# Performance work log

Measured on AMD Instinct MI355X. Metric: run time of the kernel, lower is better.

## Reference

```python
import jax, jax.numpy as jnp
import numpy as np

NUM_EXPERTS = 8
TOP_K = 2
N_EMBD = 1024
FF_HIDDEN = 4096


def setup_inputs() -> dict:
    key = jax.random.key(0)
    ks = jax.random.split(key, 5)
    scale = 0.02
    inputs = jax.random.normal(ks[0], (4, 2048, N_EMBD), dtype=jnp.float32)
    # torch Linear weights: (out_features, in_features)
    wg = jax.random.normal(ks[1], (NUM_EXPERTS, N_EMBD), dtype=jnp.float32) * scale
    w1 = jax.random.normal(ks[2], (NUM_EXPERTS, FF_HIDDEN, N_EMBD), dtype=jnp.float32) * scale
    w2 = jax.random.normal(ks[3], (NUM_EXPERTS, N_EMBD, FF_HIDDEN), dtype=jnp.float32) * scale
    w3 = jax.random.normal(ks[4], (NUM_EXPERTS, FF_HIDDEN, N_EMBD), dtype=jnp.float32) * scale
    return {"inputs": inputs, "wg": wg, "w1": w1, "w2": w2, "w3": w3}


def reference(inputs, wg, w1, w2, w3):
    B, S, D = inputs.shape
    xs = inputs.reshape(-1, D)                      # [T, D]
    T = xs.shape[0]
    E = wg.shape[0]
    gate_logits = xs @ wg.T                          # [T, E]
    top_w, sel = jax.lax.top_k(gate_logits, TOP_K)   # [T, K]
    top_w = jax.nn.softmax(top_w.astype(jnp.float32), axis=-1).astype(inputs.dtype)
    # scatter top-k weights into dense per-expert combine weights [T, E]
    combine = jnp.zeros((T, E), dtype=inputs.dtype)
    combine = combine.at[jnp.arange(T)[:, None], sel].set(top_w)
    out = jnp.zeros_like(xs)
    for e in range(E):  # small fixed loop over experts (structurally distinct weights)
        h = jax.nn.silu(xs @ w1[e].T) * (xs @ w3[e].T)   # [T, H]
        out = out + combine[:, e:e + 1] * (h @ w2[e].T)  # [T, D]
    return out.reshape(B, S, D)
```

## Files before the change

### kernel.cpp

```cpp
#include <hip/hip_runtime.h>
#include <math.h>

#define NEXP 8
#define TTOK 8192
#define DEMB 1024
#define HFF  4096

#define OFF_CNT   0
#define OFF_OFFS  64
#define OFF_PTOK  1024
#define OFF_PW    (OFF_PTOK + NEXP*TTOK*4)
#define OFF_XB    (OFF_PW + NEXP*TTOK*4)
#define OFF_WB    (OFF_XB + (size_t)TTOK*DEMB*2)

typedef short bf16x8 __attribute__((ext_vector_type(8)));
typedef float f32x4 __attribute__((ext_vector_type(4)));

__device__ __forceinline__ unsigned short f2bf(float f) {
  union { float f; unsigned int u; } v; v.f = f;
  unsigned int r = v.u + 0x7fffu + ((v.u >> 16) & 1u);
  return (unsigned short)(r >> 16);
}

__device__ __forceinline__ void gll16(const void* g, void* l) {
  __builtin_amdgcn_global_load_lds(
      (const __attribute__((address_space(1))) unsigned int*)g,
      (__attribute__((address_space(3))) unsigned int*)l, 16, 0, 0);
}

__global__ void k_convert_w(const float* __restrict__ w, uint4* __restrict__ wb) {
  size_t i = (size_t)blockIdx.x * 256 + threadIdx.x;
  float4 a = ((const float4*)w)[2 * i];
  float4 b = ((const float4*)w)[2 * i + 1];
  uint4 o;
  o.x = (unsigned)f2bf(a.x) | ((unsigned)f2bf(a.y) << 16);
  o.y = (unsigned)f2bf(a.z) | ((unsigned)f2bf(a.w) << 16);
  o.z = (unsigned)f2bf(b.x) | ((unsigned)f2bf(b.y) << 16);
  o.w = (unsigned)f2bf(b.z) | ((unsigned)f2bf(b.w) << 16);
  wb[i] = o;
}

__global__ __launch_bounds__(256) void k_gate(
    const float* __restrict__ x, const float* __restrict__ wg,
    int* __restrict__ cnt, int* __restrict__ ptok, float* __restrict__ pw,
    unsigned short* __restrict__ xb) {
  __shared__ float wgs[NEXP * DEMB];
  int tid = threadIdx.x;
  for (int i = tid; i < NEXP * DEMB / 4; i += 256)
    ((float4*)wgs)[i] = ((const float4*)wg)[i];
  __syncthreads();
  int lane = tid & 63;
  int t = blockIdx.x * 4 + (tid >> 6);
  const float* xr = x + (size_t)t * DEMB;
  unsigned short* xbr = xb + (size_t)t * DEMB;
  float acc[NEXP];
#pragma unroll
  for (int e = 0; e < NEXP; ++e) acc[e] = 0.f;
#pragma unroll
  for (int j = 0; j < 4; ++j) {
    int d = j * 256 + lane * 4;
    float4 v = *(const float4*)(xr + d);
    ushort4 o;
    o.x = f2bf(v.x); o.y = f2bf(v.y); o.z = f2bf(v.z); o.w = f2bf(v.w);
    *(ushort4*)(xbr + d) = o;
#pragma unroll
    for (int e = 0; e < NEXP; ++e) {
      float4 w = *(const float4*)(wgs + e * DEMB + d);
      acc[e] += v.x * w.x + v.y * w.y + v.z * w.z + v.w * w.w;
    }
  }
#pragma unroll
  for (int e = 0; e < NEXP; ++e) {
#pragma unroll
    for (int off = 32; off > 0; off >>= 1) acc[e] += __shfl_xor(acc[e], off);
  }
  if (lane == 0) {
    float b0 = -1e30f; int i0 = 0;
#pragma unroll
    for (int e = 0; e < NEXP; ++e) if (acc[e] > b0) { b0 = acc[e]; i0 = e; }
    float b1 = -1e30f; int i1 = 0;
#pragma unroll
    for (int e = 0; e < NEXP; ++e) if (e != i0 && acc[e] > b1) { b1 = acc[e]; i1 = e; }
    float ex = expf(b1 - b0);
    float s  = 1.f + ex;
    float w0 = 1.f / s;
    float w1v = ex / s;
    int s0 = atomicAdd(&cnt[i0], 1);
    ptok[i0 * TTOK + s0] = t; pw[i0 * TTOK + s0] = w0;
    int s1 = atomicAdd(&cnt[i1], 1);
    ptok[i1 * TTOK + s1] = t; pw[i1 * TTOK + s1] = w1v;
  }
}

__global__ void k_scan(const int* __restrict__ cnt, int* __restrict__ offs) {
  if (threadIdx.x == 0) {
    int s = 0;
    for (int e = 0; e < NEXP; ++e) { offs[e] = s; s += cnt[e]; }
  }
}


__global__ __launch_bounds__(256, 2) void k_gemm1(
    const unsigned short* __restrict__ Xb, const unsigned short* __restrict__ w1b,
    const unsigned short* __restrict__ w3b, const int* __restrict__ cnt,
    const int* __restrict__ offs, const int* __restrict__ ptok,
    unsigned short* __restrict__ Hb, int e_sel, int mbase, int mTiles) {
  int nwg = gridDim.x;
  int orig = blockIdx.x;
  int idp = (orig & 7) * (nwg >> 3) + (orig >> 3);
  int mt, e, nt;
  if (e_sel >= 0) { e = e_sel; mt = idp % mTiles; nt = idp / mTiles; }
  else { mt = idp % mTiles; e = (idp / mTiles) % NEXP; nt = idp / (mTiles * NEXP); }
  int ce = cnt[e];
  int m0 = mbase + mt * 128;
  if (m0 >= ce) return;
  int n0 = nt * 128;
  int hb = (e_sel >= 0) ? -mbase : offs[e];
  size_t eo = (size_t)((e_sel >= 0) ? 0 : e) * HFF * DEMB;
  const unsigned short* w1e = w1b + eo;
  const unsigned short* w3e = w3b + eo;

  __shared__ __align__(16) unsigned char sm[49152];
  unsigned char* As = sm;
  unsigned char* B1 = sm + 16384;
  unsigned char* B3 = sm + 32768;

  int tid = threadIdx.x, lane = tid & 63, wid = tid >> 6;
  int wm = (wid >> 1) * 64, wn = (wid & 1) * 64;

  const unsigned short *as[4], *b1s[4], *b3s[4];
#pragma unroll
  for (int it = 0; it < 4; ++it) {
    int c = it * 256 + tid;
    int row = c >> 3;
    int col = ((c & 7) ^ (row & 7)) * 8;
    int slot = m0 + row; slot = slot < ce ? slot : ce - 1;
    int tok = ptok[e * TTOK + slot];
    as[it]  = Xb + (size_t)tok * DEMB + col;
    b1s[it] = w1e + (size_t)(n0 + row) * DEMB + col;
    b3s[it] = w3e + (size_t)(n0 + row) * DEMB + col;
  }

  const f32x4 zf = {0.f, 0.f, 0.f, 0.f};
  f32x4 au[4][4], av[4][4];
#pragma unroll
  for (int a = 0; a < 4; ++a)
#pragma unroll
    for (int b = 0; b < 4; ++b) { au[a][b] = zf; av[a][b] = zf; }

  for (int kt = 0; kt < DEMB / 64; ++kt) {
    int k0 = kt * 64;
#pragma unroll
    for (int it = 0; it < 4; ++it) gll16(as[it] + k0,  As + it * 4096 + wid * 1024);
#pragma unroll
    for (int it = 0; it < 4; ++it) gll16(b1s[it] + k0, B1 + it * 4096 + wid * 1024);
#pragma unroll
    for (int it = 0; it < 4; ++it) gll16(b3s[it] + k0, B3 + it * 4096 + wid * 1024);
    __syncthreads();
#pragma unroll
    for (int kk = 0; kk < 64; kk += 32) {
      bf16x8 af[4], b1f[4], b3f[4];
      int kg = (kk >> 3) + (lane >> 4);
#pragma unroll
      for (int mr = 0; mr < 4; ++mr) {
        int r = wm + mr * 16 + (lane & 15);
        af[mr] = *(const bf16x8*)(As + r * 128 + ((kg ^ (r & 7)) * 16));
      }
#pragma unroll
      for (int nr = 0; nr < 4; ++nr) {
        int c = wn + nr * 16 + (lane & 15);
        int boff = c * 128 + ((kg ^ (c & 7)) * 16);
        b1f[nr] = *(const bf16x8*)(B1 + boff);
        b3f[nr] = *(const bf16x8*)(B3 + boff);
      }
#pragma unroll
      for (int mr = 0; mr < 4; ++mr)
#pragma unroll
        for (int nr = 0; nr < 4; ++nr) {
          au[mr][nr] = __builtin_amdgcn_mfma_f32_16x16x32_bf16(af[mr], b1f[nr], au[mr][nr], 0, 0, 0);
          av[mr][nr] = __builtin_amdgcn_mfma_f32_16x16x32_bf16(af[mr], b3f[nr], av[mr][nr], 0, 0, 0);
        }
    }
    __syncthreads();
  }
#pragma unroll
  for (int mr = 0; mr < 4; ++mr) {
#pragma unroll
    for (int j = 0; j < 4; ++j) {
      int rs = m0 + wm + mr * 16 + (lane >> 4) * 4 + j;
      if (rs < ce) {
        unsigned short* hrow = Hb + (size_t)(hb + rs) * HFF + n0 + wn + (lane & 15);
#pragma unroll
        for (int nr = 0; nr < 4; ++nr) {
          float u = au[mr][nr][j], v = av[mr][nr][j];
          float h = v * (u / (1.f + __expf(-u)));
          hrow[nr * 16] = f2bf(h);
        }
      }
    }
  }
}

__global__ __launch_bounds__(256, 2) void k_gemm2(
    const unsigned short* __restrict__ Hb, const unsigned short* __restrict__ w2b,
    const int* __restrict__ cnt, const int* __restrict__ offs,
    const int* __restrict__ ptok, const float* __restrict__ pw,
    float* __restrict__ out, int e_sel, int mbase, int mTiles) {
  int nwg = gridDim.x;
  int orig = blockIdx.x;
  int idp = (orig & 7) * (nwg >> 3) + (orig >> 3);
  int mt, e, nt;
  if (e_sel >= 0) { e = e_sel; mt = idp % mTiles; nt = idp / mTiles; }
  else { mt = idp % mTiles; e = (idp / mTiles) % NEXP; nt = idp / (mTiles * NEXP); }
  int ce = cnt[e];
  int m0 = mbase + mt * 128;
  if (m0 >= ce) return;
  int n0 = nt * 128;
  int hb = (e_sel >= 0) ? -mbase : offs[e];
  size_t eo = (size_t)((e_sel >= 0) ? 0 : e) * DEMB * HFF;
  const unsigned short* w2e = w2b + eo;

  __shared__ __align__(16) unsigned char sm[32768];
  unsigned char* As = sm;
  unsigned char* B2 = sm + 16384;

  int tid = threadIdx.x, lane = tid & 63, wid = tid >> 6;
  int wm = (wid >> 1) * 64, wn = (wid & 1) * 64;

  const unsigned short *as[4], *b2s[4];
#pragma unroll
  for (int it = 0; it < 4; ++it) {
    int c = it * 256 + tid;
    int row = c >> 3;
    int col = ((c & 7) ^ (row & 7)) * 8;
    int slot = m0 + row; slot = slot < ce ? slot : ce - 1;
    as[it]  = Hb + (size_t)(hb + slot) * HFF + col;
    b2s[it] = w2e + (size_t)(n0 + row) * HFF + col;
  }

  const f32x4 zf = {0.f, 0.f, 0.f, 0.f};
  f32x4 acc[4][4];
#pragma unroll
  for (int a = 0; a < 4; ++a)
#pragma unroll
    for (int b = 0; b < 4; ++b) acc[a][b] = zf;

  for (int kt = 0; kt < HFF / 64; ++kt) {
    int k0 = kt * 64;
#pragma unroll
    for (int it = 0; it < 4; ++it) gll16(as[it] + k0,  As + it * 4096 + wid * 1024);
#pragma unroll
    for (int it = 0; it < 4; ++it) gll16(b2s[it] + k0, B2 + it * 4096 + wid * 1024);
    __syncthreads();
#pragma unroll
    for (int kk = 0; kk < 64; kk += 32) {
      bf16x8 af[4], bf_[4];
      int kg = (kk >> 3) + (lane >> 4);
#pragma unroll
      for (int mr = 0; mr < 4; ++mr) {
        int r = wm + mr * 16 + (lane & 15);
        af[mr] = *(const bf16x8*)(As + r * 128 + ((kg ^ (r & 7)) * 16));
      }
#pragma unroll
      for (int nr = 0; nr < 4; ++nr) {
        int c = wn + nr * 16 + (lane & 15);
        bf_[nr] = *(const bf16x8*)(B2 + c * 128 + ((kg ^ (c & 7)) * 16));
      }
#pragma unroll
      for (int mr = 0; mr < 4; ++mr)
#pragma unroll
        for (int nr = 0; nr < 4; ++nr)
          acc[mr][nr] = __builtin_amdgcn_mfma_f32_16x16x32_bf16(af[mr], bf_[nr], acc[mr][nr], 0, 0, 0);
    }
    __syncthreads();
  }
#pragma unroll
  for (int mr = 0; mr < 4; ++mr) {
#pragma unroll
    for (int j = 0; j < 4; ++j) {
      int rs = m0 + wm + mr * 16 + (lane >> 4) * 4 + j;
      if (rs < ce) {
        int tok = ptok[e * TTOK + rs];
        float gw = pw[e * TTOK + rs];
        float* orow = out + (size_t)tok * DEMB + n0 + wn + (lane & 15);
#pragma unroll
        for (int nr = 0; nr < 4; ++nr)
          atomicAdd(orow + nr * 16, acc[mr][nr][j] * gw);
      }
    }
  }
}

extern "C" void kernel_launch(void* const* d_in, const int* in_sizes, int n_in,
                              void* d_out, int out_size, void* d_ws, size_t ws_size,
                              hipStream_t stream) {
  const float* x  = (const float*)d_in[0];
  const float* wg = (const float*)d_in[1];
  const float* w1 = (const float*)d_in[2];
  const float* w2 = (const float*)d_in[3];
  const float* w3 = (const float*)d_in[4];
  char* ws = (char*)d_ws;
  int*   cnt  = (int*)(ws + OFF_CNT);
  int*   offs = (int*)(ws + OFF_OFFS);
  int*   ptok = (int*)(ws + OFF_PTOK);
  float* pw   = (float*)(ws + OFF_PW);
  unsigned short* Xb = (unsigned short*)(ws + OFF_XB);
  float* out = (float*)d_out;

  const size_t WPE = (size_t)HFF * DEMB;
  hipMemsetAsync(ws + OFF_CNT, 0, 256, stream);
  hipMemsetAsync(d_out, 0, (size_t)out_size * sizeof(float), stream);
  k_gate<<<TTOK / 4, 256, 0, stream>>>(x, wg, cnt, ptok, pw, Xb);
  k_scan<<<1, 64, 0, stream>>>(cnt, offs);

  size_t needA = OFF_WB + 3 * NEXP * WPE * 2 + (size_t)2 * TTOK * HFF * 2;
  if (ws_size >= needA) {
    unsigned short* w1b = (unsigned short*)(ws + OFF_WB);
    unsigned short* w3b = w1b + NEXP * WPE;
    unsigned short* w2b = w3b + NEXP * WPE;
    unsigned short* Hb  = w2b + NEXP * WPE;
    int cgrid = (int)(NEXP * WPE / 8 / 256);
    k_convert_w<<<cgrid, 256, 0, stream>>>(w1, (uint4*)w1b);
    k_convert_w<<<cgrid, 256, 0, stream>>>(w3, (uint4*)w3b);
    k_convert_w<<<cgrid, 256, 0, stream>>>(w2, (uint4*)w2b);
    k_gemm1<<<NEXP * 64 * 32, 256, 0, stream>>>(Xb, w1b, w3b, cnt, offs, ptok, Hb, -1, 0, 64);
    k_gemm2<<<NEXP * 64 * 8, 256, 0, stream>>>(Hb, w2b, cnt, offs, ptok, pw, out, -1, 0, 64);
  } else {
    unsigned short* w1b = (unsigned short*)(ws + OFF_WB);
    unsigned short* w3b = w1b + WPE;
    unsigned short* w2b = w3b + WPE;
    unsigned short* Hb  = w2b + WPE;
    size_t offHbC = OFF_WB + 3 * WPE * 2;
    long long hbRows = ((long long)ws_size - (long long)offHbC) / (HFF * 2);
    int chunkTiles = (int)(hbRows / 128);
    if (chunkTiles < 1) chunkTiles = 1;
    if (chunkTiles > 64) chunkTiles = 64;
    int cgrid = (int)(WPE / 8 / 256);
    for (int e = 0; e < NEXP; ++e) {
      k_convert_w<<<cgrid, 256, 0, stream>>>(w1 + e * WPE, (uint4*)w1b);
      k_convert_w<<<cgrid, 256, 0, stream>>>(w3 + e * WPE, (uint4*)w3b);
      k_convert_w<<<cgrid, 256, 0, stream>>>(w2 + e * WPE, (uint4*)w2b);
      for (int mb = 0; mb < TTOK; mb += chunkTiles * 128) {
        int mT = chunkTiles;
        if (mb + mT * 128 > TTOK) mT = (TTOK - mb) / 128;
        if (mT < 1) break;
        k_gemm1<<<mT * 32, 256, 0, stream>>>(Xb, w1b, w3b, cnt, offs, ptok, Hb, e, mb, mT);
        k_gemm2<<<mT * 8, 256, 0, stream>>>(Hb, w2b, cnt, offs, ptok, pw, out, e, mb, mT);
      }
    }
  }
}
```

Baseline: 1.135 ms.

## Triple-buffer LDS pipeline with 256x128 tiles and 512-thread blocks in expert GEMMs

Both expert GEMMs move from single-buffered 128x128 tiles with 256 threads to 256-row tiles with 512 threads and a three-stage LDS ring filled by global_load_lds. Global loads for tile t+2 are issued between two compute phases, gated by manual vmcnt/lgkmcnt waits, and MFMA sections are raised with s_setprio. In gemm1 the w1 and w3 rows are interleaved into one B tile so each wave computes matching gate and up columns. This is meant to hide memory latency and cut per-iteration barrier stalls, at the cost of 144KB LDS per block, which likely limits occupancy to one block per CU.

```diff
diff --git a/kernel.cpp b/kernel.cpp
--- a/kernel.cpp
+++ b/kernel.cpp
@@ -15,6 +15,8 @@
 
 typedef short bf16x8 __attribute__((ext_vector_type(8)));
 typedef float f32x4 __attribute__((ext_vector_type(4)));
+
+#define BUFB 49152
 
 __device__ __forceinline__ unsigned short f2bf(float f) {
   union { float f; unsigned int u; } v; v.f = f;
@@ -83,12 +85,10 @@
     for (int e = 0; e < NEXP; ++e) if (e != i0 && acc[e] > b1) { b1 = acc[e]; i1 = e; }
     float ex = expf(b1 - b0);
     float s  = 1.f + ex;
-    float w0 = 1.f / s;
-    float w1v = ex / s;
     int s0 = atomicAdd(&cnt[i0], 1);
-    ptok[i0 * TTOK + s0] = t; pw[i0 * TTOK + s0] = w0;
+    ptok[i0 * TTOK + s0] = t; pw[i0 * TTOK + s0] = 1.f / s;
     int s1 = atomicAdd(&cnt[i1], 1);
-    ptok[i1 * TTOK + s1] = t; pw[i1 * TTOK + s1] = w1v;
+    ptok[i1 * TTOK + s1] = t; pw[i1 * TTOK + s1] = ex / s;
   }
 }
 
@@ -99,8 +99,14 @@
   }
 }
 
-
-__global__ __launch_bounds__(256, 2) void k_gemm1(
+#define GATE6()  { asm volatile("s_waitcnt vmcnt(6)" ::: "memory"); \
+                   __builtin_amdgcn_s_barrier(); __builtin_amdgcn_sched_barrier(0); }
+#define GATE0()  { asm volatile("s_waitcnt vmcnt(0)" ::: "memory"); \
+                   __builtin_amdgcn_s_barrier(); __builtin_amdgcn_sched_barrier(0); }
+#define LGKM0()  { asm volatile("s_waitcnt lgkmcnt(0)" ::: "memory"); \
+                   __builtin_amdgcn_sched_barrier(0); }
+
+__global__ __launch_bounds__(512, 2) void k_gemm1(
     const unsigned short* __restrict__ Xb, const unsigned short* __restrict__ w1b,
     const unsigned short* __restrict__ w3b, const int* __restrict__ cnt,
     const int* __restrict__ offs, const int* __restrict__ ptok,
@@ -112,96 +118,132 @@
   if (e_sel >= 0) { e = e_sel; mt = idp % mTiles; nt = idp / mTiles; }
   else { mt = idp % mTiles; e = (idp / mTiles) % NEXP; nt = idp / (mTiles * NEXP); }
   int ce = cnt[e];
-  int m0 = mbase + mt * 128;
+  int m0 = mbase + mt * 256;
   if (m0 >= ce) return;
-  int n0 = nt * 128;
+  int h0 = nt * 64;
   int hb = (e_sel >= 0) ? -mbase : offs[e];
   size_t eo = (size_t)((e_sel >= 0) ? 0 : e) * HFF * DEMB;
   const unsigned short* w1e = w1b + eo;
   const unsigned short* w3e = w3b + eo;
 
-  __shared__ __align__(16) unsigned char sm[49152];
-  unsigned char* As = sm;
-  unsigned char* B1 = sm + 16384;
-  unsigned char* B3 = sm + 32768;
-
+  __shared__ __align__(16) unsigned char sm[3 * BUFB];
   int tid = threadIdx.x, lane = tid & 63, wid = tid >> 6;
-  int wm = (wid >> 1) * 64, wn = (wid & 1) * 64;
-
-  const unsigned short *as[4], *b1s[4], *b3s[4];
-#pragma unroll
-  for (int it = 0; it < 4; ++it) {
-    int c = it * 256 + tid;
-    int row = c >> 3;
-    int col = ((c & 7) ^ (row & 7)) * 8;
+  int wm = wid >> 2, wn = wid & 3;
+
+  const unsigned short* sA[4];
+#pragma unroll
+  for (int i = 0; i < 4; ++i) {
+    int c = i * 512 + tid;
+    int row = c >> 3, g = c & 7;
     int slot = m0 + row; slot = slot < ce ? slot : ce - 1;
     int tok = ptok[e * TTOK + slot];
-    as[it]  = Xb + (size_t)tok * DEMB + col;
-    b1s[it] = w1e + (size_t)(n0 + row) * DEMB + col;
-    b3s[it] = w3e + (size_t)(n0 + row) * DEMB + col;
-  }
+    sA[i] = Xb + (size_t)tok * DEMB + ((g ^ (row & 7)) * 8);
+  }
+  const unsigned short* sB[2];
+#pragma unroll
+  for (int i = 0; i < 2; ++i) {
+    int c = i * 512 + tid;
+    int br = c >> 3, g = c & 7;
+    int wn_ = br >> 5, cc = br & 15, mat = (br >> 4) & 1;
+    int hr = h0 + wn_ * 16 + cc;
+    const unsigned short* wsrc = mat ? w3e : w1e;
+    sB[i] = wsrc + (size_t)hr * DEMB + ((g ^ (br & 7)) * 8);
+  }
+
+#define G1_STAGE_P0(pb, tt) { size_t o = (size_t)(tt) * 64; \
+    gll16(sA[0] + o, sm + (pb) * BUFB + 0 * 8192 + wid * 1024); \
+    gll16(sA[1] + o, sm + (pb) * BUFB + 1 * 8192 + wid * 1024); \
+    gll16(sA[2] + o, sm + (pb) * BUFB + 2 * 8192 + wid * 1024); }
+#define G1_STAGE_P1(pb, tt) { size_t o = (size_t)(tt) * 64; \
+    gll16(sA[3] + o, sm + (pb) * BUFB + 3 * 8192 + wid * 1024); \
+    gll16(sB[0] + o, sm + (pb) * BUFB + 32768 + wid * 1024); \
+    gll16(sB[1] + o, sm + (pb) * BUFB + 32768 + 8192 + wid * 1024); }
 
   const f32x4 zf = {0.f, 0.f, 0.f, 0.f};
-  f32x4 au[4][4], av[4][4];
-#pragma unroll
-  for (int a = 0; a < 4; ++a)
-#pragma unroll
-    for (int b = 0; b < 4; ++b) { au[a][b] = zf; av[a][b] = zf; }
-
-  for (int kt = 0; kt < DEMB / 64; ++kt) {
-    int k0 = kt * 64;
-#pragma unroll
-    for (int it = 0; it < 4; ++it) gll16(as[it] + k0,  As + it * 4096 + wid * 1024);
-#pragma unroll
-    for (int it = 0; it < 4; ++it) gll16(b1s[it] + k0, B1 + it * 4096 + wid * 1024);
-#pragma unroll
-    for (int it = 0; it < 4; ++it) gll16(b3s[it] + k0, B3 + it * 4096 + wid * 1024);
-    __syncthreads();
-#pragma unroll
-    for (int kk = 0; kk < 64; kk += 32) {
-      bf16x8 af[4], b1f[4], b3f[4];
-      int kg = (kk >> 3) + (lane >> 4);
-#pragma unroll
-      for (int mr = 0; mr < 4; ++mr) {
-        int r = wm + mr * 16 + (lane & 15);
-        af[mr] = *(const bf16x8*)(As + r * 128 + ((kg ^ (r & 7)) * 16));
-      }
-#pragma unroll
-      for (int nr = 0; nr < 4; ++nr) {
-        int c = wn + nr * 16 + (lane & 15);
-        int boff = c * 128 + ((kg ^ (c & 7)) * 16);
-        b1f[nr] = *(const bf16x8*)(B1 + boff);
-        b3f[nr] = *(const bf16x8*)(B3 + boff);
-      }
-#pragma unroll
-      for (int mr = 0; mr < 4; ++mr)
-#pragma unroll
-        for (int nr = 0; nr < 4; ++nr) {
-          au[mr][nr] = __builtin_amdgcn_mfma_f32_16x16x32_bf16(af[mr], b1f[nr], au[mr][nr], 0, 0, 0);
-          av[mr][nr] = __builtin_amdgcn_mfma_f32_16x16x32_bf16(af[mr], b3f[nr], av[mr][nr], 0, 0, 0);
-        }
-    }
-    __syncthreads();
-  }
-#pragma unroll
-  for (int mr = 0; mr < 4; ++mr) {
+  f32x4 acc[8][2];
+#pragma unroll
+  for (int a = 0; a < 8; ++a) { acc[a][0] = zf; acc[a][1] = zf; }
+
+  const int NT = DEMB / 64;
+  G1_STAGE_P0(0, 0) G1_STAGE_P1(0, 0)
+  G1_STAGE_P0(1, 1) G1_STAGE_P1(1, 1)
+
+  bf16x8 af[4][2], bf[2][2];
+  for (int t = 0; t < NT; ++t) {
+    if (t < NT - 1) GATE6() else GATE0()
+    const unsigned char* Ab = sm + (t % 3) * BUFB;
+    const unsigned char* Bb = Ab + 32768;
+    int pb = (t + 2) % 3;
+    bool st = (t + 2) < NT;
+#pragma unroll
+    for (int mr = 0; mr < 4; ++mr) {
+      int r = wm * 128 + mr * 16 + (lane & 15);
+#pragma unroll
+      for (int ks = 0; ks < 2; ++ks) {
+        int kg = ks * 4 + (lane >> 4);
+        af[mr][ks] = *(const bf16x8*)(Ab + r * 128 + ((kg ^ (r & 7)) * 16));
+      }
+    }
+#pragma unroll
+    for (int nr = 0; nr < 2; ++nr) {
+      int br = wn * 32 + nr * 16 + (lane & 15);
+#pragma unroll
+      for (int ks = 0; ks < 2; ++ks) {
+        int kg = ks * 4 + (lane >> 4);
+        bf[nr][ks] = *(const bf16x8*)(Bb + br * 128 + ((kg ^ (br & 7)) * 16));
+      }
+    }
+    if (st) G1_STAGE_P0(pb, t + 2)
+    LGKM0()
+    __builtin_amdgcn_s_setprio(1);
+#pragma unroll
+    for (int mr = 0; mr < 4; ++mr)
+#pragma unroll
+      for (int nr = 0; nr < 2; ++nr)
+#pragma unroll
+        for (int ks = 0; ks < 2; ++ks)
+          acc[mr][nr] = __builtin_amdgcn_mfma_f32_16x16x32_bf16(af[mr][ks], bf[nr][ks], acc[mr][nr], 0, 0, 0);
+    __builtin_amdgcn_s_setprio(0);
+    __builtin_amdgcn_s_barrier();
+#pragma unroll
+    for (int mr = 0; mr < 4; ++mr) {
+      int r = wm * 128 + 64 + mr * 16 + (lane & 15);
+#pragma unroll
+      for (int ks = 0; ks < 2; ++ks) {
+        int kg = ks * 4 + (lane >> 4);
+        af[mr][ks] = *(const bf16x8*)(Ab + r * 128 + ((kg ^ (r & 7)) * 16));
+      }
+    }
+    if (st) G1_STAGE_P1(pb, t + 2)
+    LGKM0()
+    __builtin_amdgcn_s_setprio(1);
+#pragma unroll
+    for (int mr = 0; mr < 4; ++mr)
+#pragma unroll
+      for (int nr = 0; nr < 2; ++nr)
+#pragma unroll
+        for (int ks = 0; ks < 2; ++ks)
+          acc[4 + mr][nr] = __builtin_amdgcn_mfma_f32_16x16x32_bf16(af[mr][ks], bf[nr][ks], acc[4 + mr][nr], 0, 0, 0);
+    __builtin_amdgcn_s_setprio(0);
+  }
+  int col = h0 + wn * 16 + (lane & 15);
+#pragma unroll
+  for (int mr = 0; mr < 8; ++mr) {
 #pragma unroll
     for (int j = 0; j < 4; ++j) {
-      int rs = m0 + wm + mr * 16 + (lane >> 4) * 4 + j;
+      int rs = m0 + wm * 128 + mr * 16 + (lane >> 4) * 4 + j;
       if (rs < ce) {
-        unsigned short* hrow = Hb + (size_t)(hb + rs) * HFF + n0 + wn + (lane & 15);
-#pragma unroll
-        for (int nr = 0; nr < 4; ++nr) {
-          float u = au[mr][nr][j], v = av[mr][nr][j];
-          float h = v * (u / (1.f + __expf(-u)));
-          hrow[nr * 16] = f2bf(h);
-        }
-      }
-    }
-  }
-}
-
-__global__ __launch_bounds__(256, 2) void k_gemm2(
+        float u = acc[mr][0][j], v = acc[mr][1][j];
+        float h = v * (u / (1.f + __expf(-u)));
+        Hb[(size_t)(hb + rs) * HFF + col] = f2bf(h);
+      }
+    }
+  }
+#undef G1_STAGE_P0
+#undef G1_STAGE_P1
+}
+
+__global__ __launch_bounds__(512, 2) void k_gemm2(
     const unsigned short* __restrict__ Hb, const unsigned short* __restrict__ w2b,
     const int* __restrict__ cnt, const int* __restrict__ offs,
     const int* __restrict__ ptok, const float* __restrict__ pw,
@@ -213,82 +255,126 @@
   if (e_sel >= 0) { e = e_sel; mt = idp % mTiles; nt = idp / mTiles; }
   else { mt = idp % mTiles; e = (idp / mTiles) % NEXP; nt = idp / (mTiles * NEXP); }
   int ce = cnt[e];
-  int m0 = mbase + mt * 128;
+  int m0 = mbase + mt * 256;
   if (m0 >= ce) return;
   int n0 = nt * 128;
   int hb = (e_sel >= 0) ? -mbase : offs[e];
   size_t eo = (size_t)((e_sel >= 0) ? 0 : e) * DEMB * HFF;
   const unsigned short* w2e = w2b + eo;
 
-  __shared__ __align__(16) unsigned char sm[32768];
-  unsigned char* As = sm;
-  unsigned char* B2 = sm + 16384;
-
+  __shared__ __align__(16) unsigned char sm[3 * BUFB];
   int tid = threadIdx.x, lane = tid & 63, wid = tid >> 6;
-  int wm = (wid >> 1) * 64, wn = (wid & 1) * 64;
-
-  const unsigned short *as[4], *b2s[4];
-#pragma unroll
-  for (int it = 0; it < 4; ++it) {
-    int c = it * 256 + tid;
-    int row = c >> 3;
-    int col = ((c & 7) ^ (row & 7)) * 8;
+  int wm = wid >> 2, wn = wid & 3;
+
+  const unsigned short* sA[4];
+#pragma unroll
+  for (int i = 0; i < 4; ++i) {
+    int c = i * 512 + tid;
+    int row = c >> 3, g = c & 7;
     int slot = m0 + row; slot = slot < ce ? slot : ce - 1;
-    as[it]  = Hb + (size_t)(hb + slot) * HFF + col;
-    b2s[it] = w2e + (size_t)(n0 + row) * HFF + col;
-  }
+    sA[i] = Hb + (size_t)(hb + slot) * HFF + ((g ^ (row & 7)) * 8);
+  }
+  const unsigned short* sB[2];
+#pragma unroll
+  for (int i = 0; i < 2; ++i) {
+    int c = i * 512 + tid;
+    int br = c >> 3, g = c & 7;
+    sB[i] = w2e + (size_t)(n0 + br) * HFF + ((g ^ (br & 7)) * 8);
+  }
+
+#define G2_STAGE_P0(pb, tt) { size_t o = (size_t)(tt) * 64; \
+    gll16(sA[0] + o, sm + (pb) * BUFB + 0 * 8192 + wid * 1024); \
+    gll16(sA[1] + o, sm + (pb) * BUFB + 1 * 8192 + wid * 1024); \
+    gll16(sA[2] + o, sm + (pb) * BUFB + 2 * 8192 + wid * 1024); }
+#define G2_STAGE_P1(pb, tt) { size_t o = (size_t)(tt) * 64; \
+    gll16(sA[3] + o, sm + (pb) * BUFB + 3 * 8192 + wid * 1024); \
+    gll16(sB[0] + o, sm + (pb) * BUFB + 32768 + wid * 1024); \
+    gll16(sB[1] + o, sm + (pb) * BUFB + 32768 + 8192 + wid * 1024); }
 
   const f32x4 zf = {0.f, 0.f, 0.f, 0.f};
-  f32x4 acc[4][4];
-#pragma unroll
-  for (int a = 0; a < 4; ++a)
-#pragma unroll
-    for (int b = 0; b < 4; ++b) acc[a][b] = zf;
-
-  for (int kt = 0; kt < HFF / 64; ++kt) {
-    int k0 = kt * 64;
-#pragma unroll
-    for (int it = 0; it < 4; ++it) gll16(as[it] + k0,  As + it * 4096 + wid * 1024);
-#pragma unroll
-    for (int it = 0; it < 4; ++it) gll16(b2s[it] + k0, B2 + it * 4096 + wid * 1024);
-    __syncthreads();
-#pragma unroll
-    for (int kk = 0; kk < 64; kk += 32) {
-      bf16x8 af[4], bf_[4];
-      int kg = (kk >> 3) + (lane >> 4);
-#pragma unroll
-      for (int mr = 0; mr < 4; ++mr) {
-        int r = wm + mr * 16 + (lane & 15);
-        af[mr] = *(const bf16x8*)(As + r * 128 + ((kg ^ (r & 7)) * 16));
-      }
-#pragma unroll
-      for (int nr = 0; nr < 4; ++nr) {
-        int c = wn + nr * 16 + (lane & 15);
-        bf_[nr] = *(const bf16x8*)(B2 + c * 128 + ((kg ^ (c & 7)) * 16));
-      }
-#pragma unroll
-      for (int mr = 0; mr < 4; ++mr)
-#pragma unroll
-        for (int nr = 0; nr < 4; ++nr)
-          acc[mr][nr] = __builtin_amdgcn_mfma_f32_16x16x32_bf16(af[mr], bf_[nr], acc[mr][nr], 0, 0, 0);
-    }
-    __syncthreads();
-  }
-#pragma unroll
-  for (int mr = 0; mr < 4; ++mr) {
+  f32x4 acc[8][2];
+#pragma unroll
+  for (int a = 0; a < 8; ++a) { acc[a][0] = zf; acc[a][1] = zf; }
+
+  const int NT = HFF / 64;
+  G2_STAGE_P0(0, 0) G2_STAGE_P1(0, 0)
+  G2_STAGE_P0(1, 1) G2_STAGE_P1(1, 1)
+
+  bf16x8 af[4][2], bf[2][2];
+  for (int t = 0; t < NT; ++t) {
+    if (t < NT - 1) GATE6() else GATE0()
+    const unsigned char* Ab = sm + (t % 3) * BUFB;
+    const unsigned char* Bb = Ab + 32768;
+    int pb = (t + 2) % 3;
+    bool st = (t + 2) < NT;
+#pragma unroll
+    for (int mr = 0; mr < 4; ++mr) {
+      int r = wm * 128 + mr * 16 + (lane & 15);
+#pragma unroll
+      for (int ks = 0; ks < 2; ++ks) {
+        int kg = ks * 4 + (lane >> 4);
+        af[mr][ks] = *(const bf16x8*)(Ab + r * 128 + ((kg ^ (r & 7)) * 16));
+      }
+    }
+#pragma unroll
+    for (int nr = 0; nr < 2; ++nr) {
+      int br = wn * 32 + nr * 16 + (lane & 15);
+#pragma unroll
+      for (int ks = 0; ks < 2; ++ks) {
+        int kg = ks * 4 + (lane >> 4);
+        bf[nr][ks] = *(const bf16x8*)(Bb + br * 128 + ((kg ^ (br & 7)) * 16));
+      }
+    }
+    if (st) G2_STAGE_P0(pb, t + 2)
+    LGKM0()
+    __builtin_amdgcn_s_setprio(1);
+#pragma unroll
+    for (int mr = 0; mr < 4; ++mr)
+#pragma unroll
+      for (int nr = 0; nr < 2; ++nr)
+#pragma unroll
+        for (int ks = 0; ks < 2; ++ks)
+          acc[mr][nr] = __builtin_amdgcn_mfma_f32_16x16x32_bf16(af[mr][ks], bf[nr][ks], acc[mr][nr], 0, 0, 0);
+    __builtin_amdgcn_s_setprio(0);
+    __builtin_amdgcn_s_barrier();
+#pragma unroll
+    for (int mr = 0; mr < 4; ++mr) {
+      int r = wm * 128 + 64 + mr * 16 + (lane & 15);
+#pragma unroll
+      for (int ks = 0; ks < 2; ++ks) {
+        int kg = ks * 4 + (lane >> 4);
+        af[mr][ks] = *(const bf16x8*)(Ab + r * 128 + ((kg ^ (r & 7)) * 16));
+      }
+    }
+    if (st) G2_STAGE_P1(pb, t + 2)
+    LGKM0()
+    __builtin_amdgcn_s_setprio(1);
+#pragma unroll
+    for (int mr = 0; mr < 4; ++mr)
+#pragma unroll
+      for (int nr = 0; nr < 2; ++nr)
+#pragma unroll
+        for (int ks = 0; ks < 2; ++ks)
+          acc[4 + mr][nr] = __builtin_amdgcn_mfma_f32_16x16x32_bf16(af[mr][ks], bf[nr][ks], acc[4 + mr][nr], 0, 0, 0);
+    __builtin_amdgcn_s_setprio(0);
+  }
+#pragma unroll
+  for (int mr = 0; mr < 8; ++mr) {
 #pragma unroll
     for (int j = 0; j < 4; ++j) {
-      int rs = m0 + wm + mr * 16 + (lane >> 4) * 4 + j;
+      int rs = m0 + wm * 128 + mr * 16 + (lane >> 4) * 4 + j;
       if (rs < ce) {
         int tok = ptok[e * TTOK + rs];
         float gw = pw[e * TTOK + rs];
-        float* orow = out + (size_t)tok * DEMB + n0 + wn + (lane & 15);
-#pragma unroll
-        for (int nr = 0; nr < 4; ++nr)
+        float* orow = out + (size_t)tok * DEMB + n0 + wn * 32 + (lane & 15);
+#pragma unroll
+        for (int nr = 0; nr < 2; ++nr)
           atomicAdd(orow + nr * 16, acc[mr][nr][j] * gw);
       }
     }
   }
+#undef G2_STAGE_P0
+#undef G2_STAGE_P1
 }
 
 extern "C" void kernel_launch(void* const* d_in, const int* in_sizes, int n_in,
@@ -323,8 +409,8 @@
     k_convert_w<<<cgrid, 256, 0, stream>>>(w1, (uint4*)w1b);
     k_convert_w<<<cgrid, 256, 0, stream>>>(w3, (uint4*)w3b);
     k_convert_w<<<cgrid, 256, 0, stream>>>(w2, (uint4*)w2b);
-    k_gemm1<<<NEXP * 64 * 32, 256, 0, stream>>>(Xb, w1b, w3b, cnt, offs, ptok, Hb, -1, 0, 64);
-    k_gemm2<<<NEXP * 64 * 8, 256, 0, stream>>>(Hb, w2b, cnt, offs, ptok, pw, out, -1, 0, 64);
+    k_gemm1<<<NEXP * 32 * 64, 512, 0, stream>>>(Xb, w1b, w3b, cnt, offs, ptok, Hb, -1, 0, 32);
+    k_gemm2<<<NEXP * 32 * 8, 512, 0, stream>>>(Hb, w2b, cnt, offs, ptok, pw, out, -1, 0, 32);
   } else {
     unsigned short* w1b = (unsigned short*)(ws + OFF_WB);
     unsigned short* w3b = w1b + WPE;
@@ -332,21 +418,21 @@
     unsigned short* Hb  = w2b + WPE;
     size_t offHbC = OFF_WB + 3 * WPE * 2;
     long long hbRows = ((long long)ws_size - (long long)offHbC) / (HFF * 2);
-    int chunkTiles = (int)(hbRows / 128);
+    int chunkTiles = (int)(hbRows / 256);
     if (chunkTiles < 1) chunkTiles = 1;
-    if (chunkTiles > 64) chunkTiles = 64;
+    if (chunkTiles > 32) chunkTiles = 32;
     int cgrid = (int)(WPE / 8 / 256);
     for (int e = 0; e < NEXP; ++e) {
       k_convert_w<<<cgrid, 256, 0, stream>>>(w1 + e * WPE, (uint4*)w1b);
       k_convert_w<<<cgrid, 256, 0, stream>>>(w3 + e * WPE, (uint4*)w3b);
       k_convert_w<<<cgrid, 256, 0, stream>>>(w2 + e * WPE, (uint4*)w2b);
-      for (int mb = 0; mb < TTOK; mb += chunkTiles * 128) {
+      for (int mb = 0; mb < TTOK; mb += chunkTiles * 256) {
         int mT = chunkTiles;
-        if (mb + mT * 128 > TTOK) mT = (TTOK - mb) / 128;
+        if (mb + mT * 256 > TTOK) mT = (TTOK - mb) / 256;
         if (mT < 1) break;
-        k_gemm1<<<mT * 32, 256, 0, stream>>>(Xb, w1b, w3b, cnt, offs, ptok, Hb, e, mb, mT);
-        k_gemm2<<<mT * 8, 256, 0, stream>>>(Hb, w2b, cnt, offs, ptok, pw, out, e, mb, mT);
-      }
-    }
-  }
-}
+        k_gemm1<<<mT * 64, 512, 0, stream>>>(Xb, w1b, w3b, cnt, offs, ptok, Hb, e, mb, mT);
+        k_gemm2<<<mT * 8, 512, 0, stream>>>(Hb, w2b, cnt, offs, ptok, pw, out, e, mb, mT);
+      }
+    }
+  }
+}
```

New measurement: 1.194 ms. 1.05x slower.

## Replace atomic scatter in down-projection with per-slot stores and gather-combine kernel

Applied to the files above, without the earlier changes.

The second GEMM now writes weighted per-slot outputs into a scratch buffer (reusing the w1 bf16 region, which is dead after the first GEMM), and a new combine kernel sums each token's two expert rows into the output. Gate records each token's slot ids to drive this gather. This drops the float atomics and the output memset, and reorders the gemm2 tile mapping so the N tile varies fastest. The cost is an extra write and read of a T*K*D float buffer and one more launch.

```diff
diff --git a/kernel.cpp b/kernel.cpp
--- a/kernel.cpp
+++ b/kernel.cpp
@@ -1,5 +1,6 @@
 #include <hip/hip_runtime.h>
 #include <math.h>
+
 
 #define NEXP 8
 #define TTOK 8192
@@ -10,7 +11,8 @@
 #define OFF_OFFS  64
 #define OFF_PTOK  1024
 #define OFF_PW    (OFF_PTOK + NEXP*TTOK*4)
-#define OFF_XB    (OFF_PW + NEXP*TTOK*4)
+#define OFF_SID   (OFF_PW + NEXP*TTOK*4)
+#define OFF_XB    (OFF_SID + TTOK*2*4)
 #define OFF_WB    (OFF_XB + (size_t)TTOK*DEMB*2)
 
 typedef short bf16x8 __attribute__((ext_vector_type(8)));
@@ -43,7 +45,7 @@
 __global__ __launch_bounds__(256) void k_gate(
     const float* __restrict__ x, const float* __restrict__ wg,
     int* __restrict__ cnt, int* __restrict__ ptok, float* __restrict__ pw,
-    unsigned short* __restrict__ xb) {
+    int* __restrict__ sid, unsigned short* __restrict__ xb) {
   __shared__ float wgs[NEXP * DEMB];
   int tid = threadIdx.x;
   for (int i = tid; i < NEXP * DEMB / 4; i += 256)
@@ -83,12 +85,12 @@
     for (int e = 0; e < NEXP; ++e) if (e != i0 && acc[e] > b1) { b1 = acc[e]; i1 = e; }
     float ex = expf(b1 - b0);
     float s  = 1.f + ex;
-    float w0 = 1.f / s;
-    float w1v = ex / s;
     int s0 = atomicAdd(&cnt[i0], 1);
-    ptok[i0 * TTOK + s0] = t; pw[i0 * TTOK + s0] = w0;
+    ptok[i0 * TTOK + s0] = t; pw[i0 * TTOK + s0] = 1.f / s;
     int s1 = atomicAdd(&cnt[i1], 1);
-    ptok[i1 * TTOK + s1] = t; pw[i1 * TTOK + s1] = w1v;
+    ptok[i1 * TTOK + s1] = t; pw[i1 * TTOK + s1] = ex / s;
+    sid[2 * t]     = i0 * TTOK + s0;
+    sid[2 * t + 1] = i1 * TTOK + s1;
   }
 }
 
@@ -99,6 +101,19 @@
   }
 }
 
+__global__ void k_combine(const float* __restrict__ Ob, const int* __restrict__ sid,
+                          const int* __restrict__ offs, float* __restrict__ out) {
+  int idx = blockIdx.x * 256 + threadIdx.x;
+  int t  = idx >> 8;
+  int c4 = idx & 255;
+  int s0 = sid[2 * t], s1 = sid[2 * t + 1];
+  int r0 = offs[s0 / TTOK] + (s0 & (TTOK - 1));
+  int r1 = offs[s1 / TTOK] + (s1 & (TTOK - 1));
+  float4 a = ((const float4*)(Ob + (size_t)r0 * DEMB))[c4];
+  float4 b = ((const float4*)(Ob + (size_t)r1 * DEMB))[c4];
+  float4 o = {a.x + b.x, a.y + b.y, a.z + b.z, a.w + b.w};
+  ((float4*)(out + (size_t)t * DEMB))[c4] = o;
+}
 
 __global__ __launch_bounds__(256, 2) void k_gemm1(
     const unsigned short* __restrict__ Xb, const unsigned short* __restrict__ w1b,
@@ -205,13 +220,16 @@
     const unsigned short* __restrict__ Hb, const unsigned short* __restrict__ w2b,
     const int* __restrict__ cnt, const int* __restrict__ offs,
     const int* __restrict__ ptok, const float* __restrict__ pw,
-    float* __restrict__ out, int e_sel, int mbase, int mTiles) {
+    float* __restrict__ out, float* __restrict__ Ob,
+    int e_sel, int mbase, int mTiles) {
   int nwg = gridDim.x;
   int orig = blockIdx.x;
   int idp = (orig & 7) * (nwg >> 3) + (orig >> 3);
-  int mt, e, nt;
-  if (e_sel >= 0) { e = e_sel; mt = idp % mTiles; nt = idp / mTiles; }
-  else { mt = idp % mTiles; e = (idp / mTiles) % NEXP; nt = idp / (mTiles * NEXP); }
+  int nt = idp & 7;
+  int r  = idp >> 3;
+  int mt, e;
+  if (e_sel >= 0) { e = e_sel; mt = r; }
+  else { mt = r % mTiles; e = r / mTiles; }
   int ce = cnt[e];
   int m0 = mbase + mt * 128;
   if (m0 >= ce) return;
@@ -258,8 +276,8 @@
       int kg = (kk >> 3) + (lane >> 4);
 #pragma unroll
       for (int mr = 0; mr < 4; ++mr) {
-        int r = wm + mr * 16 + (lane & 15);
-        af[mr] = *(const bf16x8*)(As + r * 128 + ((kg ^ (r & 7)) * 16));
+        int r2 = wm + mr * 16 + (lane & 15);
+        af[mr] = *(const bf16x8*)(As + r2 * 128 + ((kg ^ (r2 & 7)) * 16));
       }
 #pragma unroll
       for (int nr = 0; nr < 4; ++nr) {
@@ -280,12 +298,17 @@
     for (int j = 0; j < 4; ++j) {
       int rs = m0 + wm + mr * 16 + (lane >> 4) * 4 + j;
       if (rs < ce) {
-        int tok = ptok[e * TTOK + rs];
         float gw = pw[e * TTOK + rs];
-        float* orow = out + (size_t)tok * DEMB + n0 + wn + (lane & 15);
-#pragma unroll
-        for (int nr = 0; nr < 4; ++nr)
-          atomicAdd(orow + nr * 16, acc[mr][nr][j] * gw);
+        if (Ob) {
+          float* orow = Ob + (size_t)(hb + rs) * DEMB + n0 + wn + (lane & 15);
+#pragma unroll
+          for (int nr = 0; nr < 4; ++nr) orow[nr * 16] = acc[mr][nr][j] * gw;
+        } else {
+          int tok = ptok[e * TTOK + rs];
+          float* orow = out + (size_t)tok * DEMB + n0 + wn + (lane & 15);
+#pragma unroll
+          for (int nr = 0; nr < 4; ++nr) atomicAdd(orow + nr * 16, acc[mr][nr][j] * gw);
+        }
       }
     }
   }
@@ -304,13 +327,13 @@
   int*   offs = (int*)(ws + OFF_OFFS);
   int*   ptok = (int*)(ws + OFF_PTOK);
   float* pw   = (float*)(ws + OFF_PW);
+  int*   sid  = (int*)(ws + OFF_SID);
   unsigned short* Xb = (unsigned short*)(ws + OFF_XB);
   float* out = (float*)d_out;
 
   const size_t WPE = (size_t)HFF * DEMB;
   hipMemsetAsync(ws + OFF_CNT, 0, 256, stream);
-  hipMemsetAsync(d_out, 0, (size_t)out_size * sizeof(float), stream);
-  k_gate<<<TTOK / 4, 256, 0, stream>>>(x, wg, cnt, ptok, pw, Xb);
+  k_gate<<<TTOK / 4, 256, 0, stream>>>(x, wg, cnt, ptok, pw, sid, Xb);
   k_scan<<<1, 64, 0, stream>>>(cnt, offs);
 
   size_t needA = OFF_WB + 3 * NEXP * WPE * 2 + (size_t)2 * TTOK * HFF * 2;
@@ -319,13 +342,16 @@
     unsigned short* w3b = w1b + NEXP * WPE;
     unsigned short* w2b = w3b + NEXP * WPE;
     unsigned short* Hb  = w2b + NEXP * WPE;
+    float* Ob = (float*)w1b;
     int cgrid = (int)(NEXP * WPE / 8 / 256);
     k_convert_w<<<cgrid, 256, 0, stream>>>(w1, (uint4*)w1b);
     k_convert_w<<<cgrid, 256, 0, stream>>>(w3, (uint4*)w3b);
     k_convert_w<<<cgrid, 256, 0, stream>>>(w2, (uint4*)w2b);
     k_gemm1<<<NEXP * 64 * 32, 256, 0, stream>>>(Xb, w1b, w3b, cnt, offs, ptok, Hb, -1, 0, 64);
-    k_gemm2<<<NEXP * 64 * 8, 256, 0, stream>>>(Hb, w2b, cnt, offs, ptok, pw, out, -1, 0, 64);
+    k_gemm2<<<NEXP * 64 * 8, 256, 0, stream>>>(Hb, w2b, cnt, offs, ptok, pw, out, Ob, -1, 0, 64);
+    k_combine<<<TTOK * (DEMB / 4) / 256, 256, 0, stream>>>(Ob, sid, offs, out);
   } else {
+    hipMemsetAsync(d_out, 0, (size_t)out_size * sizeof(float), stream);
     unsigned short* w1b = (unsigned short*)(ws + OFF_WB);
     unsigned short* w3b = w1b + WPE;
     unsigned short* w2b = w3b + WPE;
@@ -345,8 +371,8 @@
         if (mb + mT * 128 > TTOK) mT = (TTOK - mb) / 128;
         if (mT < 1) break;
         k_gemm1<<<mT * 32, 256, 0, stream>>>(Xb, w1b, w3b, cnt, offs, ptok, Hb, e, mb, mT);
-        k_gemm2<<<mT * 8, 256, 0, stream>>>(Hb, w2b, cnt, offs, ptok, pw, out, e, mb, mT);
-      }
-    }
-  }
-}
+        k_gemm2<<<mT * 8, 256, 0, stream>>>(Hb, w2b, cnt, offs, ptok, pw, out, (float*)0, e, mb, mT);
+      }
+    }
+  }
+}
```

After: 1.100 ms. 1.03x faster.
